# Performance work log

Hardware: AMD Instinct MI355X
Metric: run time of the kernel (lower is better)

Reference implementation:

```python
import jax, jax.numpy as jnp
import numpy as np

N_NODES = 50000
N_EDGES = 800000
IN_DIM = 128
NUM_HEADS = 8
OUT_DIM = 16  # per-head dim; NUM_HEADS*OUT_DIM == IN_DIM


def setup_inputs() -> dict:
    key = jax.random.key(0)
    ks = jax.random.split(key, 9)
    s = 1.0 / np.sqrt(IN_DIM)
    return {
        "h": jax.random.normal(ks[0], (N_NODES, IN_DIM), dtype=jnp.float32),
        "src": jax.random.randint(ks[1], (N_EDGES,), 0, N_NODES),
        "dst": jax.random.randint(ks[2], (N_EDGES,), 0, N_NODES),
        "WQ": jax.random.normal(ks[3], (IN_DIM, NUM_HEADS * OUT_DIM), dtype=jnp.float32) * s,
        "bQ": jnp.zeros((NUM_HEADS * OUT_DIM,), dtype=jnp.float32),
        "WK": jax.random.normal(ks[4], (IN_DIM, NUM_HEADS * OUT_DIM), dtype=jnp.float32) * s,
        "bK": jnp.zeros((NUM_HEADS * OUT_DIM,), dtype=jnp.float32),
        "WV": jax.random.normal(ks[5], (IN_DIM, NUM_HEADS * OUT_DIM), dtype=jnp.float32) * s,
        "bV": jnp.zeros((NUM_HEADS * OUT_DIM,), dtype=jnp.float32),
    }


def reference(h, src, dst, WQ, bQ, WK, bK, WV, bV):
    N = h.shape[0]
    # node projections -> [N, H, D]
    Q = (h @ WQ + bQ).reshape(N, NUM_HEADS, OUT_DIM)
    K = (h @ WK + bK).reshape(N, NUM_HEADS, OUT_DIM)
    V = (h @ WV + bV).reshape(N, NUM_HEADS, OUT_DIM)
    # edge-wise score: (K_src * Q_dst) summed over D, scaled by sqrt(D)
    inv_scale = 1.0 / np.sqrt(OUT_DIM)
    score = jnp.einsum("ehd,ehd->eh", K[src], Q[dst]) * inv_scale  # [E, H]
    score_soft = jnp.exp(jnp.clip(score, -5.0, 5.0))[..., None]    # [E, H, 1]
    # scatter-sum messages to destination nodes
    wV = jax.ops.segment_sum(V[src] * score_soft, dst, num_segments=N)  # [N, H, D]
    z = jax.ops.segment_sum(score_soft, dst, num_segments=N)            # [N, H, 1]
    return wV / (z + 1e-6)
```

## Files before the change

kernel.cpp:

```cpp
#include <hip/hip_runtime.h>
#include <hip/hip_bf16.h>

#define IN_DIM 128
#define NUM_HEADS 8
#define OUT_DIM 16

#define BKT_SHIFT 9
#define BKT_MASK 511
#define NB_MAX 128
#define SLAB_SHIFT 14

typedef unsigned int uint;
typedef unsigned short ushort;
using short8 = __attribute__((ext_vector_type(8))) short;
using f32x4  = __attribute__((ext_vector_type(4))) float;
using u32x2  = __attribute__((ext_vector_type(2))) uint;

__device__ inline uint bf16_rne(float x) {
    uint u = __float_as_uint(x);
    return (u + 0x7fffu + ((u >> 16) & 1u)) >> 16;
}

__global__ __launch_bounds__(256) void stage_wtrans(const int* __restrict__ src,
                                                    const int* __restrict__ dst,
                                                    int* __restrict__ bucketCursor,
                                                    uint* __restrict__ slab,
                                                    const float* __restrict__ WQ,
                                                    const float* __restrict__ WK,
                                                    const float* __restrict__ WV,
                                                    ushort* __restrict__ WT,
                                                    int nEdges, int nb, int sb) {
    const int t = threadIdx.x;

    if ((int)blockIdx.x >= sb) {
        int tid = (blockIdx.x - sb) * 256 + t;
        if (tid >= 384 * 16) return;
        int n = tid >> 4;
        int kg = tid & 15;
        const float* W = (n < 128) ? WQ : (n < 256) ? WK : WV;
        int c = n & 127;
        short8 o;
        #pragma unroll
        for (int j = 0; j < 8; ++j) {
            float v = W[(kg * 8 + j) * 128 + c];
            o[j] = (short)bf16_rne(v);
        }
        *(short8*)(WT + (size_t)n * 128 + kg * 8) = o;
        return;
    }

    __shared__ int cnt[4][NB_MAX];
    __shared__ int base[4][NB_MAX];
    const int wv = t >> 6;
    const int e0 = blockIdx.x * 4096;

    for (int i = t; i < 4 * NB_MAX; i += 256) ((int*)cnt)[i] = 0;
    __syncthreads();

    int myDst[16], mySrc[16];
    #pragma unroll
    for (int i = 0; i < 4; ++i) {
        int e = e0 + (i * 256 + t) * 4;
        if (e + 3 < nEdges) {
            int4 d4 = *(const int4*)(dst + e);
            int4 s4 = *(const int4*)(src + e);
            myDst[4*i+0] = d4.x; myDst[4*i+1] = d4.y; myDst[4*i+2] = d4.z; myDst[4*i+3] = d4.w;
            mySrc[4*i+0] = s4.x; mySrc[4*i+1] = s4.y; mySrc[4*i+2] = s4.z; mySrc[4*i+3] = s4.w;
        } else {
            #pragma unroll
            for (int k = 0; k < 4; ++k) {
                int ee = e + k;
                myDst[4*i+k] = (ee < nEdges) ? dst[ee] : -1;
                mySrc[4*i+k] = (ee < nEdges) ? src[ee] : 0;
            }
        }
    }
    #pragma unroll
    for (int i = 0; i < 16; ++i)
        if (myDst[i] >= 0) atomicAdd(&cnt[wv][myDst[i] >> BKT_SHIFT], 1);
    __syncthreads();

    if (t < NB_MAX) {
        int c0 = cnt[0][t], c1 = cnt[1][t], c2 = cnt[2][t], c3 = cnt[3][t];
        int tot = c0 + c1 + c2 + c3;
        int gbase = (t < nb && tot > 0) ? atomicAdd(&bucketCursor[t], tot) : 0;
        base[0][t] = gbase;
        base[1][t] = gbase + c0;
        base[2][t] = gbase + c0 + c1;
        base[3][t] = gbase + c0 + c1 + c2;
    }
    __syncthreads();
    for (int i = t; i < 4 * NB_MAX; i += 256) ((int*)cnt)[i] = 0;
    __syncthreads();

    #pragma unroll
    for (int i = 0; i < 16; ++i) {
        int d = myDst[i];
        if (d >= 0) {
            int b = d >> BKT_SHIFT;
            int pos = base[wv][b] + atomicAdd(&cnt[wv][b], 1);
            if (pos < (1 << SLAB_SHIFT))
                slab[((size_t)b << SLAB_SHIFT) + pos] = (uint)mySrc[i] | ((uint)(d & BKT_MASK) << 17);
        }
    }
}

__global__ __launch_bounds__(256) void bucket_sort(const uint* __restrict__ slab,
                                                   const int* __restrict__ bucketCursor,
                                                   int* __restrict__ offsets,
                                                   int* __restrict__ srcSorted,
                                                   int nNodes, int nEdges, int nb) {
    __shared__ int cnt[512];
    __shared__ int wsum[4];
    __shared__ int sOutBase;
    const int b = blockIdx.x;
    const int t = threadIdx.x;
    const int lane = t & 63;
    const int wv = t >> 6;
    const int count = bucketCursor[b];
    const uint* rec = slab + ((size_t)b << SLAB_SHIFT);

    if (t < 64) {
        int acc = 0;
        for (int i = t; i < b; i += 64) acc += bucketCursor[i];
        #pragma unroll
        for (int off = 32; off; off >>= 1) acc += __shfl_down(acc, off);
        if (t == 0) sOutBase = acc;
    }

    cnt[t] = 0; cnt[t + 256] = 0;
    __syncthreads();
    for (int i = t; i < count; i += 256)
        atomicAdd(&cnt[rec[i] >> 17], 1);
    __syncthreads();

    int c0 = cnt[2 * t], c1 = cnt[2 * t + 1];
    int s = c0 + c1;
    int x = s;
    #pragma unroll
    for (int off = 1; off < 64; off <<= 1) { int y = __shfl_up(x, off); if (lane >= off) x += y; }
    if (lane == 63) wsum[wv] = x;
    __syncthreads();
    if (t == 0) {
        int a = 0;
        #pragma unroll
        for (int w = 0; w < 4; ++w) { int tmp = wsum[w]; wsum[w] = a; a += tmp; }
    }
    __syncthreads();
    int prefix = wsum[wv] + (x - s);
    const int outBase = sOutBase;

    int node0 = b << BKT_SHIFT;
    int g0 = node0 + 2 * t, g1 = node0 + 2 * t + 1;
    if (g0 < nNodes) offsets[g0] = outBase + prefix;
    if (g1 < nNodes) offsets[g1] = outBase + prefix + c0;
    __syncthreads();
    cnt[2 * t] = prefix;
    cnt[2 * t + 1] = prefix + c0;
    __syncthreads();

    for (int i = t; i < count; i += 256) {
        uint r = rec[i];
        int pos = atomicAdd(&cnt[r >> 17], 1);
        srcSorted[outBase + pos] = (int)(r & 0x1ffff);
    }
    if (b == 0 && t == 0) offsets[nNodes] = nEdges;
}

__global__ __launch_bounds__(256, 2) void proj_mfma(const float* __restrict__ h,
                                                    const short* __restrict__ WT,
                                                    const float* __restrict__ bQ,
                                                    const float* __restrict__ bK,
                                                    const float* __restrict__ bV,
                                                    uint* __restrict__ Qout,
                                                    uint* __restrict__ KVout,
                                                    int nNodes) {
    const int t = threadIdx.x;
    const int lane = t & 63;
    const int w = t >> 6;
    const int lr = lane & 15;
    const int q = lane >> 4;
    const int node0 = blockIdx.x * 128 + (w & 1) * 64;
    const int chalf = w >> 1;

    short8 a[4][4];
    #pragma unroll
    for (int g = 0; g < 4; ++g) {
        const int row = node0 + g * 16 + lr;
        const bool ok = row < nNodes;
        #pragma unroll
        for (int ks = 0; ks < 4; ++ks) {
            short8 v = (short8)0;
            if (ok) {
                const float* p = h + (size_t)row * 128 + (ks * 4 + q) * 8;
                float4 f0 = *(const float4*)p;
                float4 f1 = *(const float4*)(p + 4);
                v[0] = (short)bf16_rne(f0.x); v[1] = (short)bf16_rne(f0.y);
                v[2] = (short)bf16_rne(f0.z); v[3] = (short)bf16_rne(f0.w);
                v[4] = (short)bf16_rne(f1.x); v[5] = (short)bf16_rne(f1.y);
                v[6] = (short)bf16_rne(f1.z); v[7] = (short)bf16_rne(f1.w);
            }
            a[g][ks] = v;
        }
    }

    const short8* WT8 = (const short8*)WT;

    #pragma unroll 1
    for (int cc = 0; cc < 4; ++cc) {
        const int c = chalf * 4 + cc;
        const int nq = c * 16 + lr;
        f32x4 aQ[4] = {{0,0,0,0},{0,0,0,0},{0,0,0,0},{0,0,0,0}};
        f32x4 aK[4] = {{0,0,0,0},{0,0,0,0},{0,0,0,0},{0,0,0,0}};
        f32x4 aV[4] = {{0,0,0,0},{0,0,0,0},{0,0,0,0},{0,0,0,0}};
        #pragma unroll
        for (int ks = 0; ks < 4; ++ks) {
            short8 bq = WT8[(size_t)nq * 16 + ks * 4 + q];
            short8 bk = WT8[(size_t)(nq + 128) * 16 + ks * 4 + q];
            short8 bv = WT8[(size_t)(nq + 256) * 16 + ks * 4 + q];
            #pragma unroll
            for (int g = 0; g < 4; ++g) {
                aQ[g] = __builtin_amdgcn_mfma_f32_16x16x32_bf16(a[g][ks], bq, aQ[g], 0, 0, 0);
                aK[g] = __builtin_amdgcn_mfma_f32_16x16x32_bf16(a[g][ks], bk, aK[g], 0, 0, 0);
                aV[g] = __builtin_amdgcn_mfma_f32_16x16x32_bf16(a[g][ks], bv, aV[g], 0, 0, 0);
            }
        }
        const float biasq = bQ[nq];
        const float biask = bK[nq];
        const float biasv = bV[nq];
        #pragma unroll
        for (int g = 0; g < 4; ++g) {
            #pragma unroll
            for (int r = 0; r < 4; ++r) {
                int node = node0 + g * 16 + q * 4 + r;
                float qval = aQ[g][r] + biasq;
                float qpart = __shfl_xor(qval, 1);
                if (node < nNodes) {
                    if ((lr & 1) == 0)
                        Qout[(size_t)node * 64 + (nq >> 1)] = bf16_rne(qval) | (bf16_rne(qpart) << 16);
                    KVout[(size_t)node * 128 + nq] =
                        bf16_rne(aK[g][r] + biask) | (bf16_rne(aV[g][r] + biasv) << 16);
                }
            }
        }
    }
}

__global__ __launch_bounds__(256) void agg_kernel(const int* __restrict__ offsets,
                                                  const int* __restrict__ srcSorted,
                                                  const uint* __restrict__ Q,
                                                  const uint4* __restrict__ KV,
                                                  float* __restrict__ out,
                                                  int nNodes) {
    int wid = (int)((blockIdx.x * (size_t)blockDim.x + threadIdx.x) >> 6);
    if (wid >= nNodes) return;
    const int lane = threadIdx.x & 63;
    const int li = lane & 31;
    const int hf = lane >> 5;
    const int beg = offsets[wid];
    const int end = offsets[wid + 1];

    u32x2 qp = __builtin_nontemporal_load((const u32x2*)(Q + (size_t)wid * 64) + li);
    f32x4 qv;
    qv.x = __uint_as_float(qp.x << 16);
    qv.y = __uint_as_float(qp.x & 0xffff0000u);
    qv.z = __uint_as_float(qp.y << 16);
    qv.w = __uint_as_float(qp.y & 0xffff0000u);

    f32x4 acc = {0.f, 0.f, 0.f, 0.f};
    float zacc = 0.f;

    auto compute = [&](uint4 u, float mask) {
        float k0 = __uint_as_float(u.x << 16), v0 = __uint_as_float(u.x & 0xffff0000u);
        float k1 = __uint_as_float(u.y << 16), v1 = __uint_as_float(u.y & 0xffff0000u);
        float k2 = __uint_as_float(u.z << 16), v2 = __uint_as_float(u.z & 0xffff0000u);
        float k3 = __uint_as_float(u.w << 16), v3 = __uint_as_float(u.w & 0xffff0000u);
        float p = k0 * qv.x + k1 * qv.y + k2 * qv.z + k3 * qv.w;
        p += __shfl_xor(p, 1);
        p += __shfl_xor(p, 2);
        float e = __expf(fminf(fmaxf(p * 0.25f, -5.0f), 5.0f)) * mask;
        acc.x += v0 * e; acc.y += v1 * e; acc.z += v2 * e; acc.w += v3 * e;
        zacc += e;
    };

    int j = beg;
    for (; j + 8 <= end; j += 8) {
        int sI[4];
        #pragma unroll
        for (int i = 0; i < 4; ++i) sI[i] = srcSorted[j + 2 * i + hf];
        uint4 u[4];
        #pragma unroll
        for (int i = 0; i < 4; ++i) u[i] = KV[(size_t)sI[i] * 32 + li];
        #pragma unroll
        for (int i = 0; i < 4; ++i) compute(u[i], 1.f);
    }
    for (; j + 2 <= end; j += 2) {
        uint4 u = KV[(size_t)srcSorted[j + hf] * 32 + li];
        compute(u, 1.f);
    }
    if (j < end) {
        uint4 u = KV[(size_t)srcSorted[j] * 32 + li];
        compute(u, hf ? 0.f : 1.f);
    }

    acc.x += __shfl_xor(acc.x, 32);
    acc.y += __shfl_xor(acc.y, 32);
    acc.z += __shfl_xor(acc.z, 32);
    acc.w += __shfl_xor(acc.w, 32);
    zacc  += __shfl_xor(zacc, 32);

    if (hf == 0) {
        float inv = 1.0f / (zacc + 1e-6f);
        f32x4 o = {acc.x * inv, acc.y * inv, acc.z * inv, acc.w * inv};
        __builtin_nontemporal_store(o, (f32x4*)(out + (size_t)wid * 128) + li);
    }
}

extern "C" void kernel_launch(void* const* d_in, const int* in_sizes, int n_in,
                              void* d_out, int out_size, void* d_ws, size_t ws_size,
                              hipStream_t stream) {
    const float* h   = (const float*)d_in[0];
    const int*   src = (const int*)d_in[1];
    const int*   dst = (const int*)d_in[2];
    const float* WQ  = (const float*)d_in[3];
    const float* bQ  = (const float*)d_in[4];
    const float* WK  = (const float*)d_in[5];
    const float* bK  = (const float*)d_in[6];
    const float* WV  = (const float*)d_in[7];
    const float* bV  = (const float*)d_in[8];

    const int nNodes = in_sizes[0] / IN_DIM;
    const int nEdges = in_sizes[1];
    const int nb = (nNodes + (1 << BKT_SHIFT) - 1) >> BKT_SHIFT;

    float* out = (float*)d_out;
    const size_t nf = (size_t)nNodes * 128;

    uint*   Qw          = (uint*)d_ws;
    uint*   KVw         = Qw + (size_t)nNodes * 64;
    ushort* WTw         = (ushort*)(KVw + nf);
    int*    bucketCursor= (int*)(WTw + 384 * 128);
    int*    offsets     = bucketCursor + NB_MAX;
    int*    srcSorted   = offsets + (nNodes + 1);
    uint*   slab        = (uint*)(srcSorted + nEdges);

    (void)hipMemsetAsync(bucketCursor, 0, NB_MAX * sizeof(int), stream);

    int sb = (nEdges + 4095) / 4096;
    stage_wtrans<<<sb + 24, 256, 0, stream>>>(src, dst, bucketCursor, slab,
                                              WQ, WK, WV, WTw, nEdges, nb, sb);
    bucket_sort<<<nb, 256, 0, stream>>>(slab, bucketCursor, offsets, srcSorted, nNodes, nEdges, nb);

    proj_mfma<<<(nNodes + 127) / 128, 256, 0, stream>>>(h, (const short*)WTw, bQ, bK, bV, Qw, KVw, nNodes);

    int aggBlocks = (nNodes * 64 + 255) / 256;
    agg_kernel<<<aggBlocks, 256, 0, stream>>>(offsets, srcSorted, Qw, (const uint4*)KVw, out, nNodes);
}
```

Baseline: 129.3 us.

## Use finer node buckets, smaller edge chunks, single-wave projection blocks

Shrinks the destination buckets from 512 to 128 nodes, which gives 391 buckets instead of 98. The bucket sort then runs many more blocks, with a simpler single-wave prefix scan, and each binning block handles 2048 edges instead of 4096. The projection kernel is split into 64-thread blocks, each covering one node group and one column half, and the aggregation now reads srcSorted with nontemporal loads. The aim is better GPU occupancy and parallelism in the sort stages, at the cost of more global bucket-cursor atomics and more launched blocks.

New measurement: 122.1 us, median of 2. -5.6%, faster.

```diff
diff --git a/kernel.cpp b/kernel.cpp
--- a/kernel.cpp
+++ b/kernel.cpp
@@ -5,10 +5,10 @@
 #define NUM_HEADS 8
 #define OUT_DIM 16
 
-#define BKT_SHIFT 9
-#define BKT_MASK 511
-#define NB_MAX 128
-#define SLAB_SHIFT 14
+#define BKT_SHIFT 7
+#define BKT_MASK 127
+#define NB_MAX 512
+#define SLAB_SHIFT 13
 
 typedef unsigned int uint;
 typedef unsigned short ushort;
@@ -52,14 +52,14 @@
     __shared__ int cnt[4][NB_MAX];
     __shared__ int base[4][NB_MAX];
     const int wv = t >> 6;
-    const int e0 = blockIdx.x * 4096;
+    const int e0 = blockIdx.x * 2048;
 
     for (int i = t; i < 4 * NB_MAX; i += 256) ((int*)cnt)[i] = 0;
     __syncthreads();
 
-    int myDst[16], mySrc[16];
+    int myDst[8], mySrc[8];
     #pragma unroll
-    for (int i = 0; i < 4; ++i) {
+    for (int i = 0; i < 2; ++i) {
         int e = e0 + (i * 256 + t) * 4;
         if (e + 3 < nEdges) {
             int4 d4 = *(const int4*)(dst + e);
@@ -76,25 +76,25 @@
         }
     }
     #pragma unroll
-    for (int i = 0; i < 16; ++i)
+    for (int i = 0; i < 8; ++i)
         if (myDst[i] >= 0) atomicAdd(&cnt[wv][myDst[i] >> BKT_SHIFT], 1);
     __syncthreads();
 
-    if (t < NB_MAX) {
-        int c0 = cnt[0][t], c1 = cnt[1][t], c2 = cnt[2][t], c3 = cnt[3][t];
+    for (int bb = t; bb < NB_MAX; bb += 256) {
+        int c0 = cnt[0][bb], c1 = cnt[1][bb], c2 = cnt[2][bb], c3 = cnt[3][bb];
         int tot = c0 + c1 + c2 + c3;
-        int gbase = (t < nb && tot > 0) ? atomicAdd(&bucketCursor[t], tot) : 0;
-        base[0][t] = gbase;
-        base[1][t] = gbase + c0;
-        base[2][t] = gbase + c0 + c1;
-        base[3][t] = gbase + c0 + c1 + c2;
+        int gbase = (bb < nb && tot > 0) ? atomicAdd(&bucketCursor[bb], tot) : 0;
+        base[0][bb] = gbase;
+        base[1][bb] = gbase + c0;
+        base[2][bb] = gbase + c0 + c1;
+        base[3][bb] = gbase + c0 + c1 + c2;
     }
     __syncthreads();
     for (int i = t; i < 4 * NB_MAX; i += 256) ((int*)cnt)[i] = 0;
     __syncthreads();
 
     #pragma unroll
-    for (int i = 0; i < 16; ++i) {
+    for (int i = 0; i < 8; ++i) {
         int d = myDst[i];
         if (d >= 0) {
             int b = d >> BKT_SHIFT;
@@ -110,53 +110,43 @@
                                                    int* __restrict__ offsets,
                                                    int* __restrict__ srcSorted,
                                                    int nNodes, int nEdges, int nb) {
-    __shared__ int cnt[512];
-    __shared__ int wsum[4];
+    __shared__ int cnt[128];
     __shared__ int sOutBase;
     const int b = blockIdx.x;
     const int t = threadIdx.x;
-    const int lane = t & 63;
-    const int wv = t >> 6;
     const int count = bucketCursor[b];
     const uint* rec = slab + ((size_t)b << SLAB_SHIFT);
 
-    if (t < 64) {
+    if (t < 128) cnt[t] = 0;
+    if (t >= 64 && t < 128) {
+        int l = t - 64;
         int acc = 0;
-        for (int i = t; i < b; i += 64) acc += bucketCursor[i];
+        for (int i = l; i < b; i += 64) acc += bucketCursor[i];
         #pragma unroll
         for (int off = 32; off; off >>= 1) acc += __shfl_down(acc, off);
-        if (t == 0) sOutBase = acc;
-    }
-
-    cnt[t] = 0; cnt[t + 256] = 0;
-    __syncthreads();
+        if (l == 0) sOutBase = acc;
+    }
+    __syncthreads();
+
     for (int i = t; i < count; i += 256)
         atomicAdd(&cnt[rec[i] >> 17], 1);
     __syncthreads();
 
-    int c0 = cnt[2 * t], c1 = cnt[2 * t + 1];
-    int s = c0 + c1;
-    int x = s;
-    #pragma unroll
-    for (int off = 1; off < 64; off <<= 1) { int y = __shfl_up(x, off); if (lane >= off) x += y; }
-    if (lane == 63) wsum[wv] = x;
-    __syncthreads();
-    if (t == 0) {
-        int a = 0;
-        #pragma unroll
-        for (int w = 0; w < 4; ++w) { int tmp = wsum[w]; wsum[w] = a; a += tmp; }
-    }
-    __syncthreads();
-    int prefix = wsum[wv] + (x - s);
     const int outBase = sOutBase;
-
-    int node0 = b << BKT_SHIFT;
-    int g0 = node0 + 2 * t, g1 = node0 + 2 * t + 1;
-    if (g0 < nNodes) offsets[g0] = outBase + prefix;
-    if (g1 < nNodes) offsets[g1] = outBase + prefix + c0;
-    __syncthreads();
-    cnt[2 * t] = prefix;
-    cnt[2 * t + 1] = prefix + c0;
+    if (t < 64) {
+        int c0 = cnt[2 * t], c1 = cnt[2 * t + 1];
+        int s = c0 + c1;
+        int x = s;
+        #pragma unroll
+        for (int off = 1; off < 64; off <<= 1) { int y = __shfl_up(x, off); if (t >= off) x += y; }
+        int prefix = x - s;
+        int node0 = b << BKT_SHIFT;
+        int g0 = node0 + 2 * t, g1 = node0 + 2 * t + 1;
+        if (g0 < nNodes) offsets[g0] = outBase + prefix;
+        if (g1 < nNodes) offsets[g1] = outBase + prefix + c0;
+        cnt[2 * t] = prefix;
+        cnt[2 * t + 1] = prefix + c0;
+    }
     __syncthreads();
 
     for (int i = t; i < count; i += 256) {
@@ -167,21 +157,19 @@
     if (b == 0 && t == 0) offsets[nNodes] = nEdges;
 }
 
-__global__ __launch_bounds__(256, 2) void proj_mfma(const float* __restrict__ h,
-                                                    const short* __restrict__ WT,
-                                                    const float* __restrict__ bQ,
-                                                    const float* __restrict__ bK,
-                                                    const float* __restrict__ bV,
-                                                    uint* __restrict__ Qout,
-                                                    uint* __restrict__ KVout,
-                                                    int nNodes) {
-    const int t = threadIdx.x;
-    const int lane = t & 63;
-    const int w = t >> 6;
+__global__ __launch_bounds__(64, 2) void proj_mfma(const float* __restrict__ h,
+                                                   const short* __restrict__ WT,
+                                                   const float* __restrict__ bQ,
+                                                   const float* __restrict__ bK,
+                                                   const float* __restrict__ bV,
+                                                   uint* __restrict__ Qout,
+                                                   uint* __restrict__ KVout,
+                                                   int nNodes) {
+    const int lane = threadIdx.x;
     const int lr = lane & 15;
     const int q = lane >> 4;
-    const int node0 = blockIdx.x * 128 + (w & 1) * 64;
-    const int chalf = w >> 1;
+    const int node0 = (blockIdx.x >> 1) * 64;
+    const int chalf = blockIdx.x & 1;
 
     short8 a[4][4];
     #pragma unroll
@@ -287,7 +275,7 @@
     for (; j + 8 <= end; j += 8) {
         int sI[4];
         #pragma unroll
-        for (int i = 0; i < 4; ++i) sI[i] = srcSorted[j + 2 * i + hf];
+        for (int i = 0; i < 4; ++i) sI[i] = __builtin_nontemporal_load(srcSorted + j + 2 * i + hf);
         uint4 u[4];
         #pragma unroll
         for (int i = 0; i < 4; ++i) u[i] = KV[(size_t)sI[i] * 32 + li];
@@ -346,12 +334,13 @@
 
     (void)hipMemsetAsync(bucketCursor, 0, NB_MAX * sizeof(int), stream);
 
-    int sb = (nEdges + 4095) / 4096;
+    int sb = (nEdges + 2047) / 2048;
     stage_wtrans<<<sb + 24, 256, 0, stream>>>(src, dst, bucketCursor, slab,
                                               WQ, WK, WV, WTw, nEdges, nb, sb);
     bucket_sort<<<nb, 256, 0, stream>>>(slab, bucketCursor, offsets, srcSorted, nNodes, nEdges, nb);
 
-    proj_mfma<<<(nNodes + 127) / 128, 256, 0, stream>>>(h, (const short*)WTw, bQ, bK, bV, Qw, KVw, nNodes);
+    int projBlocks = ((nNodes + 63) / 64) * 2;
+    proj_mfma<<<projBlocks, 64, 0, stream>>>(h, (const short*)WTw, bQ, bK, bV, Qw, KVw, nNodes);
 
     int aggBlocks = (nNodes * 64 + 255) / 256;
     agg_kernel<<<aggBlocks, 256, 0, stream>>>(offsets, srcSorted, Qw, (const uint4*)KVw, out, nNodes);
```
